# Kernel optimization log

Hardware: AMD Instinct MI355X
Metric: run time of the kernel (lower is better)

The kernel has to match this reference:

```python
import jax, jax.numpy as jnp
import numpy as np

NUM_EMBEDDINGS = 512
EMBEDDING_DIM = 64


def setup_inputs() -> dict:
    key = jax.random.key(0)
    k1, k2 = jax.random.split(key)
    z = jax.random.normal(k1, (4, EMBEDDING_DIM, 16, 64, 64), dtype=jnp.float32)
    # embedding init: uniform(-1/K, 1/K)
    bound = 1.0 / NUM_EMBEDDINGS
    emb_weight = jax.random.uniform(k2, (NUM_EMBEDDINGS, EMBEDDING_DIM),
                                    dtype=jnp.float32, minval=-bound, maxval=bound)
    return {"z": z, "emb_weight": emb_weight}


def reference(z, emb_weight):
    # z: [B, C, D, H, W] with C == embedding_dim
    B, C, D, H, W = z.shape
    z_perm = jnp.transpose(z, (0, 2, 3, 4, 1))          # [B, D, H, W, C]
    flat_z = z_perm.reshape(-1, C)                       # [N, C]
    distances = (jnp.sum(flat_z * flat_z, axis=1, keepdims=True)
                 - 2.0 * flat_z @ emb_weight.T
                 + jnp.sum(emb_weight * emb_weight, axis=1))  # [N, K]
    encoding_indices = jnp.argmin(distances, axis=1)     # [N]
    # jit-safe unique count: number of codebook entries used at least once
    counts = jnp.zeros((emb_weight.shape[0],), dtype=jnp.int32).at[encoding_indices].add(1)
    unique_codes = jnp.sum(counts > 0)
    z_q = emb_weight[encoding_indices].reshape(z_perm.shape)  # [B, D, H, W, C]
    # straight-through estimator
    z_q = z_perm + jax.lax.stop_gradient(z_q - z_perm)
    z_q = jnp.transpose(z_q, (0, 4, 1, 2, 3))            # [B, C, D, H, W]
    return z_q, unique_codes
```

## Files before the change

### kernel.cpp

```cpp
#include <hip/hip_runtime.h>
#include <hip/hip_bf16.h>

#define NPOS (4*16*64*64)
#define KCODES 512
#define CDIM 64
#define OUT_SCALAR_IDX ((size_t)NPOS * CDIM)

#define WS_GCOUNT 0
#define WS_EMB    4096
#define WS_EE     (4096 + 32768)

typedef float f32x4 __attribute__((ext_vector_type(4)));
typedef long lng2 __attribute__((ext_vector_type(2)));

__global__ __launch_bounds__(64) void vq_prep(
    const float* __restrict__ emb, char* __restrict__ ws) {
  const int r = blockIdx.x * 64 + threadIdx.x;
  ((int*)(ws + WS_GCOUNT))[r] = 0;
  float c[CDIM];
  float ee = 0.f;
  #pragma unroll
  for (int q = 0; q < 16; ++q) {
    float4 x = ((const float4*)(emb + r * CDIM))[q];
    c[4*q+0] = x.x; c[4*q+1] = x.y; c[4*q+2] = x.z; c[4*q+3] = x.w;
    ee = fmaf(x.x, x.x, ee); ee = fmaf(x.y, x.y, ee);
    ee = fmaf(x.z, x.z, ee); ee = fmaf(x.w, x.w, ee);
  }
  #pragma unroll
  for (int kg = 0; kg < 4; ++kg) {
    uint u[4];
    #pragma unroll
    for (int h = 0; h < 2; ++h)
      #pragma unroll
      for (int jj = 0; jj < 2; ++jj) {
        const int kb = h * 32 + kg * 8 + jj * 4;
        uint p = __builtin_amdgcn_cvt_pk_fp8_f32(-512.f * c[kb+0], -512.f * c[kb+1], 0u, false);
        p = __builtin_amdgcn_cvt_pk_fp8_f32(-512.f * c[kb+2], -512.f * c[kb+3], p, true);
        u[h * 2 + jj] = p;
      }
    *(uint4*)(ws + WS_EMB + kg * 8192 + r * 16) = make_uint4(u[0], u[1], u[2], u[3]);
  }
  ((float*)(ws + WS_EE))[r] = 256.f * (1.f + ee);
}

__global__ __launch_bounds__(512, 8) void vq_mfma(
    const float* __restrict__ z, const float* __restrict__ emb,
    const char* __restrict__ ws, float* __restrict__ out,
    int* __restrict__ gflags) {
  __shared__ lng2 embs[2048];
  __shared__ float s_ee[KCODES];
  __shared__ uint s_idx[256];
  __shared__ int s_hist[KCODES];

  const int tid = threadIdx.x;
  const int lane = tid & 63;
  const int w = tid >> 6;
  const int col = lane & 15;
  const int kg = lane >> 4;

  if (tid < 128)
    __builtin_amdgcn_global_load_lds(
        (const __attribute__((address_space(1))) void*)(ws + WS_EE + tid * 16),
        (__attribute__((address_space(3))) void*)((char*)s_ee + tid * 16), 16, 0, 0);
  const char* src = ws + WS_EMB;
  #pragma unroll
  for (int i = 0; i < 4; ++i) {
    const int off = (i * 512 + tid) * 16;
    __builtin_amdgcn_global_load_lds(
        (const __attribute__((address_space(1))) void*)(src + off),
        (__attribute__((address_space(3))) void*)((char*)embs + off), 16, 0, 0);
  }

  const int nb = blockIdx.x * 256;
  const int b = nb >> 16, spb = nb & 65535;
  const float* zp0 = z + ((size_t)b << 22) + spb;
  long af[2][2];
  #pragma unroll
  for (int rt = 0; rt < 2; ++rt) {
    const float* zp = zp0 + w * 32 + rt * 16 + col;
    #pragma unroll
    for (int h = 0; h < 2; ++h) {
      float v[8];
      #pragma unroll
      for (int j = 0; j < 8; ++j)
        v[j] = zp[(size_t)(h * 32 + kg * 8 + j) << 16];
      uint u0 = __builtin_amdgcn_cvt_pk_fp8_f32(v[0], v[1], 0u, false);
      u0 = __builtin_amdgcn_cvt_pk_fp8_f32(v[2], v[3], u0, true);
      uint u1 = __builtin_amdgcn_cvt_pk_fp8_f32(v[4], v[5], 0u, false);
      u1 = __builtin_amdgcn_cvt_pk_fp8_f32(v[6], v[7], u1, true);
      af[rt][h] = ((long)u1 << 32) | (long)u0;
    }
  }
  s_hist[tid] = 0;

  __syncthreads();

  uint key[2][4];
  #pragma unroll
  for (int rt = 0; rt < 2; ++rt)
    #pragma unroll
    for (int s = 0; s < 4; ++s) key[rt][s] = 0xFFFFFFFFu;

  const int lbyte = kg * 8192 + col * 16;

  lng2 bb = *(const lng2*)((const char*)embs + lbyte);
  float eev = s_ee[col];

  #pragma unroll 8
  for (int ct = 0; ct < 32; ++ct) {
    const lng2 bc = bb;
    const float ec = eev;
    const uint ctv = (uint)ct;
    const int nct = (ct + 1) & 31;
    bb = *(const lng2*)((const char*)embs + nct * 256 + lbyte);
    eev = s_ee[nct * 16 + col];
    const f32x4 cin = {ec, ec, ec, ec};
    #pragma unroll
    for (int rt = 0; rt < 2; ++rt) {
      f32x4 acc = __builtin_amdgcn_mfma_f32_16x16x32_fp8_fp8(af[rt][0], bc.x, cin, 0, 0, 0);
      acc = __builtin_amdgcn_mfma_f32_16x16x32_fp8_fp8(af[rt][1], bc.y, acc, 0, 0, 0);
      #pragma unroll
      for (int s = 0; s < 4; ++s) {
        uint kb = (__builtin_bit_cast(uint, acc[s]) & 0xFFFFFFE0u) | ctv;
        key[rt][s] = kb < key[rt][s] ? kb : key[rt][s];
      }
    }
  }

  #pragma unroll
  for (int rt = 0; rt < 2; ++rt) {
    #pragma unroll
    for (int s = 0; s < 4; ++s) {
      uint k = (key[rt][s] << 4) | (uint)col;
      #pragma unroll
      for (int m = 1; m < 16; m <<= 1) {
        uint o = (uint)__shfl_xor((int)k, m, 64);
        k = o < k ? o : k;
      }
      if (col == 0) s_idx[w * 32 + rt * 16 + kg * 4 + s] = k;
    }
  }
  __syncthreads();

  const int p = tid & 255;
  const int half = tid >> 8;
  const uint kk = s_idx[p];
  const int myidx = (int)(((kk >> 4) & 31u) * 16u + (kk & 15u));
  if (half == 0) atomicAdd(&s_hist[myidx], 1);
  {
    const float4* ef = (const float4*)(emb + myidx * CDIM + half * 32);
    float* o = out + ((size_t)b << 22) + ((size_t)(half * 32) << 16) + spb + p;
    #pragma unroll
    for (int q = 0; q < 8; ++q) {
      float4 e4 = ef[q];
      o[(size_t)(4 * q + 0) << 16] = e4.x;
      o[(size_t)(4 * q + 1) << 16] = e4.y;
      o[(size_t)(4 * q + 2) << 16] = e4.z;
      o[(size_t)(4 * q + 3) << 16] = e4.w;
    }
  }
  __syncthreads();
  if (s_hist[tid]) gflags[tid] = 1;
}

__global__ __launch_bounds__(512) void vq_count(
    const int* __restrict__ gflags, float* __restrict__ out) {
  __shared__ int red[512];
  const int t = threadIdx.x;
  red[t] = (gflags[t] > 0) ? 1 : 0;
  __syncthreads();
  for (int s = 256; s > 0; s >>= 1) {
    if (t < s) red[t] += red[t + s];
    __syncthreads();
  }
  if (t == 0) out[OUT_SCALAR_IDX] = (float)red[0];
}

extern "C" void kernel_launch(void* const* d_in, const int* in_sizes, int n_in,
                              void* d_out, int out_size, void* d_ws, size_t ws_size,
                              hipStream_t stream) {
  const float* z = (const float*)d_in[0];
  const float* emb = (const float*)d_in[1];
  float* out = (float*)d_out;
  char* ws = (char*)d_ws;
  int* gflags = (int*)(ws + WS_GCOUNT);

  vq_prep<<<8, 64, 0, stream>>>(emb, ws);
  vq_mfma<<<NPOS / 256, 512, 0, stream>>>(z, emb, ws, out, gflags);
  vq_count<<<1, 512, 0, stream>>>(gflags, out);
}
```

Measured before the change: 45.72 us.

## Process two 256-position chunks per block with prefetched z loads

Each block now handles 512 positions instead of 256, so the codebook LDS staging is amortized over twice the work. All z loads for both chunks are issued up front, and a partial vmcnt wait lets the second chunk's global loads overlap the first chunk's MFMA search. Occupancy hint drops from 8 to 4 blocks per CU because of the extra prefetch registers, and the gather/write phase now has each thread write all 64 channels for one position.

```diff
diff --git a/kernel.cpp b/kernel.cpp
--- a/kernel.cpp
+++ b/kernel.cpp
@@ -43,13 +43,13 @@
   ((float*)(ws + WS_EE))[r] = 256.f * (1.f + ee);
 }
 
-__global__ __launch_bounds__(512, 8) void vq_mfma(
+__global__ __launch_bounds__(512, 4) void vq_mfma(
     const float* __restrict__ z, const float* __restrict__ emb,
     const char* __restrict__ ws, float* __restrict__ out,
     int* __restrict__ gflags) {
   __shared__ lng2 embs[2048];
   __shared__ float s_ee[KCODES];
-  __shared__ uint s_idx[256];
+  __shared__ uint s_idx[512];
   __shared__ int s_hist[KCODES];
 
   const int tid = threadIdx.x;
@@ -71,87 +71,114 @@
         (__attribute__((address_space(3))) void*)((char*)embs + off), 16, 0, 0);
   }
 
-  const int nb = blockIdx.x * 256;
+  const int nb = blockIdx.x * 512;
   const int b = nb >> 16, spb = nb & 65535;
   const float* zp0 = z + ((size_t)b << 22) + spb;
-  long af[2][2];
-  #pragma unroll
-  for (int rt = 0; rt < 2; ++rt) {
-    const float* zp = zp0 + w * 32 + rt * 16 + col;
-    #pragma unroll
-    for (int h = 0; h < 2; ++h) {
-      float v[8];
+  const int pbase = w * 32 + col;
+
+  float pf0[32], pf1[32];
+  #pragma unroll
+  for (int rt = 0; rt < 2; ++rt)
+    #pragma unroll
+    for (int h = 0; h < 2; ++h)
       #pragma unroll
       for (int j = 0; j < 8; ++j)
-        v[j] = zp[(size_t)(h * 32 + kg * 8 + j) << 16];
-      uint u0 = __builtin_amdgcn_cvt_pk_fp8_f32(v[0], v[1], 0u, false);
-      u0 = __builtin_amdgcn_cvt_pk_fp8_f32(v[2], v[3], u0, true);
-      uint u1 = __builtin_amdgcn_cvt_pk_fp8_f32(v[4], v[5], 0u, false);
-      u1 = __builtin_amdgcn_cvt_pk_fp8_f32(v[6], v[7], u1, true);
-      af[rt][h] = ((long)u1 << 32) | (long)u0;
+        pf0[rt*16 + h*8 + j] =
+            zp0[pbase + rt*16 + ((size_t)(h*32 + kg*8 + j) << 16)];
+  #pragma unroll
+  for (int rt = 0; rt < 2; ++rt)
+    #pragma unroll
+    for (int h = 0; h < 2; ++h)
+      #pragma unroll
+      for (int j = 0; j < 8; ++j)
+        pf1[rt*16 + h*8 + j] =
+            zp0[256 + pbase + rt*16 + ((size_t)(h*32 + kg*8 + j) << 16)];
+
+  long af0[2][2];
+  #pragma unroll
+  for (int rt = 0; rt < 2; ++rt)
+    #pragma unroll
+    for (int h = 0; h < 2; ++h) {
+      const int o = rt*16 + h*8;
+      uint u0 = __builtin_amdgcn_cvt_pk_fp8_f32(pf0[o+0], pf0[o+1], 0u, false);
+      u0 = __builtin_amdgcn_cvt_pk_fp8_f32(pf0[o+2], pf0[o+3], u0, true);
+      uint u1 = __builtin_amdgcn_cvt_pk_fp8_f32(pf0[o+4], pf0[o+5], 0u, false);
+      u1 = __builtin_amdgcn_cvt_pk_fp8_f32(pf0[o+6], pf0[o+7], u1, true);
+      af0[rt][h] = ((long)u1 << 32) | (long)u0;
     }
-  }
   s_hist[tid] = 0;
 
+  asm volatile("s_waitcnt vmcnt(32) lgkmcnt(0)" ::: "memory");
+  __builtin_amdgcn_sched_barrier(0);
+  __builtin_amdgcn_s_barrier();
+  __builtin_amdgcn_sched_barrier(0);
+
+  const int lbyte = kg * 8192 + col * 16;
+
+#define CHUNK(AF, SBASE)                                                       \
+  {                                                                            \
+    uint key[2][4];                                                            \
+    _Pragma("unroll") for (int rt = 0; rt < 2; ++rt)                           \
+      _Pragma("unroll") for (int s = 0; s < 4; ++s) key[rt][s] = 0xFFFFFFFFu;  \
+    lng2 bb = *(const lng2*)((const char*)embs + lbyte);                       \
+    float eev = s_ee[col];                                                     \
+    _Pragma("unroll 8")                                                        \
+    for (int ct = 0; ct < 32; ++ct) {                                          \
+      const lng2 bc = bb;                                                      \
+      const float ec = eev;                                                    \
+      const uint ctv = (uint)ct;                                               \
+      const int nct = (ct + 1) & 31;                                           \
+      bb = *(const lng2*)((const char*)embs + nct * 256 + lbyte);              \
+      eev = s_ee[nct * 16 + col];                                              \
+      const f32x4 cin = {ec, ec, ec, ec};                                      \
+      _Pragma("unroll") for (int rt = 0; rt < 2; ++rt) {                       \
+        f32x4 acc =                                                            \
+            __builtin_amdgcn_mfma_f32_16x16x32_fp8_fp8(AF[rt][0], bc.x, cin, 0, 0, 0); \
+        acc = __builtin_amdgcn_mfma_f32_16x16x32_fp8_fp8(AF[rt][1], bc.y, acc, 0, 0, 0); \
+        _Pragma("unroll") for (int s = 0; s < 4; ++s) {                        \
+          uint kb = (__builtin_bit_cast(uint, acc[s]) & 0xFFFFFFE0u) | ctv;    \
+          key[rt][s] = kb < key[rt][s] ? kb : key[rt][s];                      \
+        }                                                                      \
+      }                                                                        \
+    }                                                                          \
+    _Pragma("unroll") for (int rt = 0; rt < 2; ++rt)                           \
+      _Pragma("unroll") for (int s = 0; s < 4; ++s) {                          \
+        uint k = (key[rt][s] << 4) | (uint)col;                                \
+        _Pragma("unroll") for (int m = 1; m < 16; m <<= 1) {                   \
+          uint o = (uint)__shfl_xor((int)k, m, 64);                            \
+          k = o < k ? o : k;                                                   \
+        }                                                                      \
+        if (col == 0) s_idx[(SBASE) + w * 32 + rt * 16 + kg * 4 + s] = k;      \
+      }                                                                        \
+  }
+
+  CHUNK(af0, 0)
+
+  long af1[2][2];
+  #pragma unroll
+  for (int rt = 0; rt < 2; ++rt)
+    #pragma unroll
+    for (int h = 0; h < 2; ++h) {
+      const int o = rt*16 + h*8;
+      uint u0 = __builtin_amdgcn_cvt_pk_fp8_f32(pf1[o+0], pf1[o+1], 0u, false);
+      u0 = __builtin_amdgcn_cvt_pk_fp8_f32(pf1[o+2], pf1[o+3], u0, true);
+      uint u1 = __builtin_amdgcn_cvt_pk_fp8_f32(pf1[o+4], pf1[o+5], 0u, false);
+      u1 = __builtin_amdgcn_cvt_pk_fp8_f32(pf1[o+6], pf1[o+7], u1, true);
+      af1[rt][h] = ((long)u1 << 32) | (long)u0;
+    }
+
+  CHUNK(af1, 256)
+
   __syncthreads();
 
-  uint key[2][4];
-  #pragma unroll
-  for (int rt = 0; rt < 2; ++rt)
-    #pragma unroll
-    for (int s = 0; s < 4; ++s) key[rt][s] = 0xFFFFFFFFu;
-
-  const int lbyte = kg * 8192 + col * 16;
-
-  lng2 bb = *(const lng2*)((const char*)embs + lbyte);
-  float eev = s_ee[col];
-
-  #pragma unroll 8
-  for (int ct = 0; ct < 32; ++ct) {
-    const lng2 bc = bb;
-    const float ec = eev;
-    const uint ctv = (uint)ct;
-    const int nct = (ct + 1) & 31;
-    bb = *(const lng2*)((const char*)embs + nct * 256 + lbyte);
-    eev = s_ee[nct * 16 + col];
-    const f32x4 cin = {ec, ec, ec, ec};
-    #pragma unroll
-    for (int rt = 0; rt < 2; ++rt) {
-      f32x4 acc = __builtin_amdgcn_mfma_f32_16x16x32_fp8_fp8(af[rt][0], bc.x, cin, 0, 0, 0);
-      acc = __builtin_amdgcn_mfma_f32_16x16x32_fp8_fp8(af[rt][1], bc.y, acc, 0, 0, 0);
-      #pragma unroll
-      for (int s = 0; s < 4; ++s) {
-        uint kb = (__builtin_bit_cast(uint, acc[s]) & 0xFFFFFFE0u) | ctv;
-        key[rt][s] = kb < key[rt][s] ? kb : key[rt][s];
-      }
-    }
-  }
-
-  #pragma unroll
-  for (int rt = 0; rt < 2; ++rt) {
-    #pragma unroll
-    for (int s = 0; s < 4; ++s) {
-      uint k = (key[rt][s] << 4) | (uint)col;
-      #pragma unroll
-      for (int m = 1; m < 16; m <<= 1) {
-        uint o = (uint)__shfl_xor((int)k, m, 64);
-        k = o < k ? o : k;
-      }
-      if (col == 0) s_idx[w * 32 + rt * 16 + kg * 4 + s] = k;
-    }
-  }
-  __syncthreads();
-
-  const int p = tid & 255;
-  const int half = tid >> 8;
-  const uint kk = s_idx[p];
+  const uint kk = s_idx[tid];
   const int myidx = (int)(((kk >> 4) & 31u) * 16u + (kk & 15u));
-  if (half == 0) atomicAdd(&s_hist[myidx], 1);
+  atomicAdd(&s_hist[myidx], 1);
   {
-    const float4* ef = (const float4*)(emb + myidx * CDIM + half * 32);
-    float* o = out + ((size_t)b << 22) + ((size_t)(half * 32) << 16) + spb + p;
-    #pragma unroll
-    for (int q = 0; q < 8; ++q) {
+    const float4* ef = (const float4*)(emb + myidx * CDIM);
+    float* o = out + ((size_t)b << 22) + spb + tid;
+    #pragma unroll
+    for (int q = 0; q < 16; ++q) {
       float4 e4 = ef[q];
       o[(size_t)(4 * q + 0) << 16] = e4.x;
       o[(size_t)(4 * q + 1) << 16] = e4.y;
@@ -186,6 +213,6 @@
   int* gflags = (int*)(ws + WS_GCOUNT);
 
   vq_prep<<<8, 64, 0, stream>>>(emb, ws);
-  vq_mfma<<<NPOS / 256, 512, 0, stream>>>(z, emb, ws, out, gflags);
+  vq_mfma<<<NPOS / 512, 512, 0, stream>>>(z, emb, ws, out, gflags);
   vq_count<<<1, 512, 0, stream>>>(gflags, out);
 }
```

New measurement: 39.28 us. 1.16x faster.

## Process 512 positions per block with pipelined z loads, register gather, bitmask histogram

Applied to the files above, without the earlier changes.

Each block now handles 512 positions (four row tiles per wave), so the codebook staging into LDS is amortised over twice the work and half as many blocks launch. Loads of z are software-pipelined through two prefetch register buffers interleaved with FP8 conversion. The result gather reads codebook rows directly from registers after the shuffle reduction, overlapping gathers with stores and dropping the shared index array. Unique-code tracking moves from a per-block histogram plus global flags to per-block bitmasks in workspace, OR-reduced and popcounted in the final kernel; the block order is swizzled. Register pressure rises (launch bounds drop to 4 blocks per CU) and fewer blocks may reduce latency hiding.

```diff
diff --git a/kernel.cpp b/kernel.cpp
--- a/kernel.cpp
+++ b/kernel.cpp
@@ -1,14 +1,14 @@
 #include <hip/hip_runtime.h>
-#include <hip/hip_bf16.h>
 
 #define NPOS (4*16*64*64)
 #define KCODES 512
 #define CDIM 64
 #define OUT_SCALAR_IDX ((size_t)NPOS * CDIM)
-
-#define WS_GCOUNT 0
-#define WS_EMB    4096
-#define WS_EE     (4096 + 32768)
+#define NBLK 512
+
+#define WS_EMB   0
+#define WS_EE    32768
+#define WS_MASK  34816
 
 typedef float f32x4 __attribute__((ext_vector_type(4)));
 typedef long lng2 __attribute__((ext_vector_type(2)));
@@ -16,7 +16,6 @@
 __global__ __launch_bounds__(64) void vq_prep(
     const float* __restrict__ emb, char* __restrict__ ws) {
   const int r = blockIdx.x * 64 + threadIdx.x;
-  ((int*)(ws + WS_GCOUNT))[r] = 0;
   float c[CDIM];
   float ee = 0.f;
   #pragma unroll
@@ -43,14 +42,12 @@
   ((float*)(ws + WS_EE))[r] = 256.f * (1.f + ee);
 }
 
-__global__ __launch_bounds__(512, 8) void vq_mfma(
+__global__ __launch_bounds__(512, 4) void vq_mfma(
     const float* __restrict__ z, const float* __restrict__ emb,
-    const char* __restrict__ ws, float* __restrict__ out,
-    int* __restrict__ gflags) {
+    char* __restrict__ ws, float* __restrict__ out) {
   __shared__ lng2 embs[2048];
   __shared__ float s_ee[KCODES];
-  __shared__ uint s_idx[256];
-  __shared__ int s_hist[KCODES];
+  __shared__ uint s_mask[16];
 
   const int tid = threadIdx.x;
   const int lane = tid & 63;
@@ -58,6 +55,8 @@
   const int col = lane & 15;
   const int kg = lane >> 4;
 
+  if (tid < 16) s_mask[tid] = 0;
+
   if (tid < 128)
     __builtin_amdgcn_global_load_lds(
         (const __attribute__((address_space(1))) void*)(ws + WS_EE + tid * 16),
@@ -71,64 +70,98 @@
         (__attribute__((address_space(3))) void*)((char*)embs + off), 16, 0, 0);
   }
 
-  const int nb = blockIdx.x * 256;
+  const int swz = (blockIdx.x & 7) * 64 + (blockIdx.x >> 3);
+  const int nb = swz * 512;
   const int b = nb >> 16, spb = nb & 65535;
-  const float* zp0 = z + ((size_t)b << 22) + spb;
-  long af[2][2];
-  #pragma unroll
-  for (int rt = 0; rt < 2; ++rt) {
-    const float* zp = zp0 + w * 32 + rt * 16 + col;
-    #pragma unroll
-    for (int h = 0; h < 2; ++h) {
-      float v[8];
+  const float* zp = z + ((size_t)b << 22) + spb + w * 64 + col;
+  const int lbyte = kg * 8192 + col * 16;
+
+  float pf0[16], pf1[16];
+  long af[4][2];
+  uint key[4][4];
+  float4 ge[2][4];
+  int gidx[2][4];
+
+#define ISSUE(PF, RT)                                                          \
+  _Pragma("unroll") for (int h = 0; h < 2; ++h)                                \
+  _Pragma("unroll") for (int j = 0; j < 8; ++j)                                \
+    PF[h*8+j] = zp[(RT)*16 + ((size_t)(h*32 + kg*8 + j) << 16)];
+
+#define CONV(PF, RT)                                                           \
+  {                                                                            \
+    uint u0 = __builtin_amdgcn_cvt_pk_fp8_f32(PF[0], PF[1], 0u, false);        \
+    u0 = __builtin_amdgcn_cvt_pk_fp8_f32(PF[2], PF[3], u0, true);              \
+    uint u1 = __builtin_amdgcn_cvt_pk_fp8_f32(PF[4], PF[5], 0u, false);        \
+    u1 = __builtin_amdgcn_cvt_pk_fp8_f32(PF[6], PF[7], u1, true);              \
+    af[RT][0] = ((long)u1 << 32) | (long)u0;                                   \
+    u0 = __builtin_amdgcn_cvt_pk_fp8_f32(PF[8], PF[9], 0u, false);             \
+    u0 = __builtin_amdgcn_cvt_pk_fp8_f32(PF[10], PF[11], u0, true);            \
+    u1 = __builtin_amdgcn_cvt_pk_fp8_f32(PF[12], PF[13], 0u, false);           \
+    u1 = __builtin_amdgcn_cvt_pk_fp8_f32(PF[14], PF[15], u1, true);            \
+    af[RT][1] = ((long)u1 << 32) | (long)u0;                                   \
+  }
+
+#define GATHER(RT, GB)                                                         \
+  _Pragma("unroll") for (int s = 0; s < 4; ++s) {                              \
+    const int id = (int)(((key[RT][s] >> 4) & 31u) * 16u + (key[RT][s] & 15u)); \
+    gidx[GB][s] = id;                                                          \
+    ge[GB][s] = ((const float4*)(emb + id * CDIM))[col];                       \
+    if (col == 0) atomicOr(&s_mask[id >> 5], 1u << (id & 31));                 \
+  }
+
+#define STORE(RT, GB)                                                          \
+  _Pragma("unroll") for (int s = 0; s < 4; ++s) {                              \
+    float* o = out + ((size_t)b << 22) + ((size_t)(col * 4) << 16)             \
+               + spb + w * 64 + (RT) * 16 + kg * 4 + s;                        \
+    o[0] = ge[GB][s].x;                                                        \
+    o[(size_t)1 << 16] = ge[GB][s].y;                                          \
+    o[(size_t)2 << 16] = ge[GB][s].z;                                          \
+    o[(size_t)3 << 16] = ge[GB][s].w;                                          \
+  }
+
+  ISSUE(pf0, 0)
+  ISSUE(pf1, 1)
+  CONV(pf0, 0)
+  ISSUE(pf0, 2)
+  CONV(pf1, 1)
+  ISSUE(pf1, 3)
+  CONV(pf0, 2)
+  CONV(pf1, 3)
+
+  __syncthreads();
+
+  #pragma unroll
+  for (int rt = 0; rt < 4; ++rt)
+    #pragma unroll
+    for (int s = 0; s < 4; ++s) key[rt][s] = 0xFFFFFFFFu;
+
+  {
+    lng2 bb = *(const lng2*)((const char*)embs + lbyte);
+    float eev = s_ee[col];
+    #pragma unroll 8
+    for (int ct = 0; ct < 32; ++ct) {
+      const lng2 bc = bb;
+      const float ec = eev;
+      const uint ctv = (uint)ct;
+      const int nct = (ct + 1) & 31;
+      bb = *(const lng2*)((const char*)embs + nct * 256 + lbyte);
+      eev = s_ee[nct * 16 + col];
+      const f32x4 cin = {ec, ec, ec, ec};
       #pragma unroll
-      for (int j = 0; j < 8; ++j)
-        v[j] = zp[(size_t)(h * 32 + kg * 8 + j) << 16];
-      uint u0 = __builtin_amdgcn_cvt_pk_fp8_f32(v[0], v[1], 0u, false);
-      u0 = __builtin_amdgcn_cvt_pk_fp8_f32(v[2], v[3], u0, true);
-      uint u1 = __builtin_amdgcn_cvt_pk_fp8_f32(v[4], v[5], 0u, false);
-      u1 = __builtin_amdgcn_cvt_pk_fp8_f32(v[6], v[7], u1, true);
-      af[rt][h] = ((long)u1 << 32) | (long)u0;
-    }
-  }
-  s_hist[tid] = 0;
-
-  __syncthreads();
-
-  uint key[2][4];
-  #pragma unroll
-  for (int rt = 0; rt < 2; ++rt)
-    #pragma unroll
-    for (int s = 0; s < 4; ++s) key[rt][s] = 0xFFFFFFFFu;
-
-  const int lbyte = kg * 8192 + col * 16;
-
-  lng2 bb = *(const lng2*)((const char*)embs + lbyte);
-  float eev = s_ee[col];
-
-  #pragma unroll 8
-  for (int ct = 0; ct < 32; ++ct) {
-    const lng2 bc = bb;
-    const float ec = eev;
-    const uint ctv = (uint)ct;
-    const int nct = (ct + 1) & 31;
-    bb = *(const lng2*)((const char*)embs + nct * 256 + lbyte);
-    eev = s_ee[nct * 16 + col];
-    const f32x4 cin = {ec, ec, ec, ec};
-    #pragma unroll
-    for (int rt = 0; rt < 2; ++rt) {
-      f32x4 acc = __builtin_amdgcn_mfma_f32_16x16x32_fp8_fp8(af[rt][0], bc.x, cin, 0, 0, 0);
-      acc = __builtin_amdgcn_mfma_f32_16x16x32_fp8_fp8(af[rt][1], bc.y, acc, 0, 0, 0);
-      #pragma unroll
-      for (int s = 0; s < 4; ++s) {
-        uint kb = (__builtin_bit_cast(uint, acc[s]) & 0xFFFFFFE0u) | ctv;
-        key[rt][s] = kb < key[rt][s] ? kb : key[rt][s];
+      for (int rt = 0; rt < 4; ++rt) {
+        f32x4 acc = __builtin_amdgcn_mfma_f32_16x16x32_fp8_fp8(af[rt][0], bc.x, cin, 0, 0, 0);
+        acc = __builtin_amdgcn_mfma_f32_16x16x32_fp8_fp8(af[rt][1], bc.y, acc, 0, 0, 0);
+        #pragma unroll
+        for (int s = 0; s < 4; ++s) {
+          uint kb = (__builtin_bit_cast(uint, acc[s]) & 0xFFFFFFE0u) | ctv;
+          key[rt][s] = kb < key[rt][s] ? kb : key[rt][s];
+        }
       }
     }
   }
 
   #pragma unroll
-  for (int rt = 0; rt < 2; ++rt) {
+  for (int rt = 0; rt < 4; ++rt)
     #pragma unroll
     for (int s = 0; s < 4; ++s) {
       uint k = (key[rt][s] << 4) | (uint)col;
@@ -137,43 +170,44 @@
         uint o = (uint)__shfl_xor((int)k, m, 64);
         k = o < k ? o : k;
       }
-      if (col == 0) s_idx[w * 32 + rt * 16 + kg * 4 + s] = k;
+      key[rt][s] = k;
     }
-  }
+
+  GATHER(0, 0)
+  GATHER(1, 1)
+  STORE(0, 0)
+  GATHER(2, 0)
+  STORE(1, 1)
+  GATHER(3, 1)
+  STORE(2, 0)
+  STORE(3, 1)
+
   __syncthreads();
-
-  const int p = tid & 255;
-  const int half = tid >> 8;
-  const uint kk = s_idx[p];
-  const int myidx = (int)(((kk >> 4) & 31u) * 16u + (kk & 15u));
-  if (half == 0) atomicAdd(&s_hist[myidx], 1);
-  {
-    const float4* ef = (const float4*)(emb + myidx * CDIM + half * 32);
-    float* o = out + ((size_t)b << 22) + ((size_t)(half * 32) << 16) + spb + p;
-    #pragma unroll
-    for (int q = 0; q < 8; ++q) {
-      float4 e4 = ef[q];
-      o[(size_t)(4 * q + 0) << 16] = e4.x;
-      o[(size_t)(4 * q + 1) << 16] = e4.y;
-      o[(size_t)(4 * q + 2) << 16] = e4.z;
-      o[(size_t)(4 * q + 3) << 16] = e4.w;
-    }
-  }
+  if (tid < 16)
+    ((uint*)(ws + WS_MASK))[blockIdx.x * 16 + tid] = s_mask[tid];
+}
+
+__global__ __launch_bounds__(512) void vq_count(
+    const char* __restrict__ ws, float* __restrict__ out) {
+  __shared__ uint red[512];
+  const int t = threadIdx.x;
+  const uint* masks = (const uint*)(ws + WS_MASK);
+  uint v = 0;
+  #pragma unroll
+  for (int g = 0; g < NBLK / 32; ++g)
+    v |= masks[((t >> 4) + g * 32) * 16 + (t & 15)];
+  red[t] = v;
   __syncthreads();
-  if (s_hist[tid]) gflags[tid] = 1;
-}
-
-__global__ __launch_bounds__(512) void vq_count(
-    const int* __restrict__ gflags, float* __restrict__ out) {
-  __shared__ int red[512];
-  const int t = threadIdx.x;
-  red[t] = (gflags[t] > 0) ? 1 : 0;
-  __syncthreads();
-  for (int s = 256; s > 0; s >>= 1) {
-    if (t < s) red[t] += red[t + s];
+  for (int s = 256; s >= 16; s >>= 1) {
+    if (t < s) red[t] |= red[t + s];
     __syncthreads();
   }
-  if (t == 0) out[OUT_SCALAR_IDX] = (float)red[0];
+  if (t == 0) {
+    int c = 0;
+    #pragma unroll
+    for (int i = 0; i < 16; ++i) c += __popc(red[i]);
+    out[OUT_SCALAR_IDX] = (float)c;
+  }
 }
 
 extern "C" void kernel_launch(void* const* d_in, const int* in_sizes, int n_in,
@@ -183,9 +217,8 @@
   const float* emb = (const float*)d_in[1];
   float* out = (float*)d_out;
   char* ws = (char*)d_ws;
-  int* gflags = (int*)(ws + WS_GCOUNT);
 
   vq_prep<<<8, 64, 0, stream>>>(emb, ws);
-  vq_mfma<<<NPOS / 256, 512, 0, stream>>>(z, emb, ws, out, gflags);
-  vq_count<<<1, 512, 0, stream>>>(gflags, out);
-}
+  vq_mfma<<<NBLK, 512, 0, stream>>>(z, emb, ws, out);
+  vq_count<<<1, 512, 0, stream>>>(ws, out);
+}
```

Measured after the change: 37.98 us. 1.2x faster.
